# Performance work log

Measured on AMD Instinct MI355X. Metric: run time of the kernel, lower is better.

Reference implementation:

```python
import jax, jax.numpy as jnp
import numpy as np

B = 8192
D = 32
K = 8
H0 = 256
H1 = 256
PER = 3 * K + 1  # 25 params per dim
SCALE = 10.0
RMIN, RMAX = -SCALE / 2.0, SCALE / 2.0
MIN_BW = 1e-3; MIN_BH = 1e-3; MIN_KS = 1e-3
CUR_STEPS = 10000.0; CUR_START = 0.0
DX_MB = 1e-4   # distrax min_bin_size default
DX_MS = 1e-4   # distrax min_knot_slope default
DX_OFF = float(np.log(np.expm1(1.0 - DX_MS)))  # so softplus(0+off)+ms == 1


def _masks():
    deg_in = np.arange(1, D + 1)
    hd0 = np.arange(H0) % (D - 1) + 1
    hd1 = np.arange(H1) % (D - 1) + 1
    m0 = (hd0[:, None] >= deg_in[None, :]).astype(np.float32).T      # (D, H0)
    m1 = (hd1[:, None] >= hd0[None, :]).astype(np.float32).T        # (H0, H1)
    out_mask = (deg_in[:, None] > hd1[None, :]).astype(np.float32)  # (D, H1)
    per_mask = np.repeat(out_mask, PER, axis=0)                      # (D*PER, H1)
    return jnp.asarray(m0), jnp.asarray(m1), jnp.asarray(per_mask)

M0, M1, PER_MASK = _masks()


def made(y, W0, b0, W1, b1, W_out, b_out):
    h = jax.nn.gelu(y @ (W0 * M0) + b0)
    h = jax.nn.gelu(h @ (W1 * M1) + b1)
    proj = h @ (W_out.T * PER_MASK.T) + b_out  # (B, D*PER)
    return proj.reshape(y.shape[0], D, PER)


def _g(a, idx):
    return jnp.take_along_axis(a, idx[..., None], axis=-1)[..., 0]


def _knots(p, training_step):
    # module-level processing (rqs_from_params) ...
    w_raw, h_raw, s_raw = p[..., :K], p[..., K:2 * K], p[..., 2 * K:]
    lw = jax.nn.softmax(w_raw, axis=-1) * SCALE * (1.0 - K * MIN_BW) + MIN_BW
    lh = jax.nn.softmax(h_raw, axis=-1) * SCALE * (1.0 - K * MIN_BH) + MIN_BH
    ls = jax.nn.softplus(s_raw) + MIN_KS
    alpha = jnp.clip((jnp.asarray(training_step, jnp.float32) - CUR_START) / CUR_STEPS, 0.0, 1.0)
    bw = (1.0 - alpha) * (SCALE / K) + alpha * lw
    bh = (1.0 - alpha) * (SCALE / K) + alpha * lh
    sl = (1.0 - alpha) * 1.0 + alpha * ls
    bw = bw / jnp.sum(bw, axis=-1, keepdims=True) * SCALE
    bh = bh / jnp.sum(bh, axis=-1, keepdims=True) * SCALE
    # ... followed by distrax.RationalQuadraticSpline internal normalization
    widths = jax.nn.softmax(bw, axis=-1) * (SCALE - K * DX_MB) + DX_MB
    heights = jax.nn.softmax(bh, axis=-1) * (SCALE - K * DX_MB) + DX_MB
    slopes = jax.nn.softplus(sl + DX_OFF) + DX_MS  # (..., K+1)
    zpad = jnp.zeros_like(widths[..., :1])
    xp = RMIN + jnp.concatenate([zpad, jnp.cumsum(widths, axis=-1)], axis=-1)
    yp = RMIN + jnp.concatenate([zpad, jnp.cumsum(heights, axis=-1)], axis=-1)
    return xp, yp, widths, heights, slopes


def spline_fwd(p, x, training_step):
    xp, yp, w, h, d = _knots(p, training_step)
    inr = (x >= RMIN) & (x <= RMAX)
    xc = jnp.clip(x, RMIN, RMAX)
    idx = jnp.clip(jnp.sum((xc[..., None] >= xp[..., :-1]), axis=-1) - 1, 0, K - 1)
    xk, yk = _g(xp, idx), _g(yp, idx)
    wk, hk = _g(w, idx), _g(h, idx)
    dk, dk1 = _g(d, idx), _g(d, idx + 1)
    s = hk / wk
    xi = (xc - xk) / wk
    z1 = xi * (1.0 - xi)
    den = s + (dk1 + dk - 2.0 * s) * z1
    y = yk + hk * (s * xi * xi + dk * z1) / den
    ld = 2.0 * jnp.log(s) + jnp.log(dk1 * xi * xi + 2.0 * s * z1 + dk * (1.0 - xi) ** 2) - 2.0 * jnp.log(den)
    return jnp.where(inr, y, x), jnp.where(inr, ld, 0.0)


def spline_inv(p, y, training_step):
    xp, yp, w, h, d = _knots(p, training_step)
    inr = (y >= RMIN) & (y <= RMAX)
    yc = jnp.clip(y, RMIN, RMAX)
    idx = jnp.clip(jnp.sum((yc[..., None] >= yp[..., :-1]), axis=-1) - 1, 0, K - 1)
    xk, yk = _g(xp, idx), _g(yp, idx)
    wk, hk = _g(w, idx), _g(h, idx)
    dk, dk1 = _g(d, idx), _g(d, idx + 1)
    s = hk / wk
    t = yc - yk
    coef = dk1 + dk - 2.0 * s
    a = hk * (s - dk) + t * coef
    b = hk * dk - t * coef
    c = -s * t
    xi = 2.0 * c / (-b - jnp.sqrt(b * b - 4.0 * a * c))
    x = xi * wk + xk
    z1 = xi * (1.0 - xi)
    den = s + coef * z1
    ld = -(2.0 * jnp.log(s) + jnp.log(dk1 * xi * xi + 2.0 * s * z1 + dk * (1.0 - xi) ** 2) - 2.0 * jnp.log(den))
    return jnp.where(inr, x, y), jnp.where(inr, ld, 0.0)


def setup_inputs() -> dict:
    ks = jax.random.split(jax.random.key(0), 4)
    sd = lambda k, shp, fan: jax.random.normal(k, shp, jnp.float32) / np.sqrt(fan).astype(np.float32)
    return {
        "x": jax.random.normal(ks[0], (B, D), jnp.float32) * 1.5,
        "W0": sd(ks[1], (D, H0), D),
        "b0": jnp.zeros((H0,), jnp.float32),
        "W1": sd(ks[2], (H0, H1), H0),
        "b1": jnp.zeros((H1,), jnp.float32),
        "W_out": sd(ks[3], (D * PER, H1), H1),
        "b_out": jnp.zeros((D * PER,), jnp.float32),
        "forward": 0,
        "training_step": 10000,
    }


def reference(x, W0, b0, W1, b1, W_out, b_out, forward, training_step):
    if forward:
        p = made(x, W0, b0, W1, b1, W_out, b_out)  # (B, D, PER)
        z, ld = spline_fwd(p, x, training_step)
        return z, jnp.sum(ld, axis=1)
    z = x

    def body(carry, i):
        x_so, ldj = carry
        p = made(x_so, W0, b0, W1, b1, W_out, b_out)
        p_i = jax.lax.dynamic_index_in_dim(p, i, axis=1, keepdims=False)  # (B, PER)
        z_i = jax.lax.dynamic_index_in_dim(z, i, axis=1, keepdims=False)  # (B,)
        x_i, ld = spline_inv(p_i, z_i, training_step)
        return (x_so.at[:, i].set(x_i), ldj + ld), None

    init = (jnp.zeros_like(z), jnp.zeros((z.shape[0],), z.dtype))
    (x_fin, ldj), _ = jax.lax.scan(body, init, jnp.arange(D))
    return x_fin, ldj
```

## Files before the change

### kernel.cpp

```cpp
#include <hip/hip_runtime.h>

typedef _Float16 f16x8 __attribute__((ext_vector_type(8)));
typedef float f32x4 __attribute__((ext_vector_type(4)));

#define NB 8192
#define DD 32
#define PER 25
#define STRH 272

#define FENCE_C() do { asm volatile("" ::: "memory"); \
                       __builtin_amdgcn_sched_barrier(0); } while (0)
#define FENCE_HW() do { asm volatile("s_waitcnt lgkmcnt(0)" ::: "memory"); \
                        __builtin_amdgcn_sched_barrier(0); } while (0)

__device__ __forceinline__ float rcp_f(float x) { return __builtin_amdgcn_rcpf(x); }
__device__ __forceinline__ float gelu_f(float x) {
    float a = -1.5957691216057308f * (x + 0.044715f * x * x * x);
    return x * rcp_f(1.0f + __expf(a));
}
__device__ __forceinline__ float softplus_f(float x) {
    return (x > 20.0f) ? x : __logf(1.0f + __expf(x));
}
__device__ __forceinline__ int cntf(int d) {
    return (d <= 0) ? 0 : ((d <= 8) ? 9 * d : 72 + 8 * (d - 8));
}
__device__ __forceinline__ int porig(int u) {
    int d = (u < 72) ? (u / 9 + 1) : ((u - 72) / 8 + 9);
    int s = (u < 72) ? (u % 9) : ((u - 72) % 8);
    return s * 31 + (d - 1);
}

template<int CTRL>
__device__ __forceinline__ float qperm(float v) {
    return __int_as_float(__builtin_amdgcn_update_dpp(
        0, __float_as_int(v), CTRL, 0xF, 0xF, true));
}
__device__ __forceinline__ float qsum2(float v) {
    v += qperm<0xB1>(v);
    v += qperm<0x4E>(v);
    return v;
}
__device__ __forceinline__ float qmax2(float v) {
    v = fmaxf(v, qperm<0xB1>(v));
    v = fmaxf(v, qperm<0x4E>(v));
    return v;
}
__device__ __forceinline__ float qscan(float v, int p) {
    float t = qperm<0x90>(v);
    float c = v + ((p >= 1) ? t : 0.0f);
    float t2 = qperm<0x44>(c);
    return c + ((p >= 2) ? t2 : 0.0f);
}
__device__ __forceinline__ float sel4(float r0, float r1, float r2, float r3, int m) {
    float lo = (m & 1) ? r1 : r0;
    float hi = (m & 1) ? r3 : r2;
    return (m & 2) ? hi : lo;
}

__global__ void prep_kernel(const float* __restrict__ W0, const float* __restrict__ b0,
                            const float* __restrict__ W1, const float* __restrict__ b1,
                            const float* __restrict__ Wout, const float* __restrict__ bout,
                            _Float16* __restrict__ W0F, _Float16* __restrict__ W1F,
                            _Float16* __restrict__ WoutF,
                            float* __restrict__ b0F, float* __restrict__ b1F,
                            float* __restrict__ boutF)
{
    const int total = 16384 + 131072 + 262144 + 512 + 512 + 1024;
    for (int e = blockIdx.x * blockDim.x + threadIdx.x; e < total;
         e += gridDim.x * blockDim.x) {
        if (e < 16384) {
            int i = e >> 9, r = e & 511, lane = r >> 3, j = r & 7;
            int c = lane & 15, k = ((lane >> 4) << 3) + j;
            int nn = cntf(i) - cntf(i - 1);
            float v = 0.0f;
            if (c < nn && k < i) v = W0[k * 256 + (c * 31 + i - 1)];
            W0F[e] = (_Float16)v;
        } else if (e < 16384 + 131072) {
            int m = e - 16384;
            int i = m >> 12, r = m & 4095, kt = r >> 9, r2 = r & 511;
            int lane = r2 >> 3, j = r2 & 7;
            int c = lane & 15, kpos = kt * 32 + ((lane >> 4) << 3) + j;
            int nn = cntf(i) - cntf(i - 1), chi = cntf(i);
            float v = 0.0f;
            if (c < nn && kpos < chi) v = W1[porig(kpos) * 256 + (c * 31 + i - 1)];
            W1F[m] = (_Float16)v;
        } else if (e < 16384 + 131072 + 262144) {
            int m = e - (16384 + 131072);
            int i = m >> 13, r = m & 8191, ct = r >> 12, r2 = r & 4095;
            int kt = r2 >> 9, r3 = r2 & 511, lane = r3 >> 3, j = r3 & 7;
            int par = ct * 16 + (lane & 15), kpos = kt * 32 + ((lane >> 4) << 3) + j;
            int chi = cntf(i);
            float v = 0.0f;
            if (par < 25 && kpos < chi) v = Wout[(i * 25 + par) * 256 + porig(kpos)];
            WoutF[m] = (_Float16)v;
        } else if (e < 409600 + 512) {
            int m = e - 409600;
            int i = m >> 4, c = m & 15;
            int nn = cntf(i) - cntf(i - 1);
            b0F[m] = (c < nn) ? b0[c * 31 + i - 1] : 0.0f;
        } else if (e < 410112 + 512) {
            int m = e - 410112;
            int i = m >> 4, c = m & 15;
            int nn = cntf(i) - cntf(i - 1);
            b1F[m] = (c < nn) ? b1[c * 31 + i - 1] : 0.0f;
        } else {
            int m = e - 410624;
            int i = m >> 5, c = m & 31;
            boutF[m] = (c < 25) ? bout[i * 25 + c] : 0.0f;
        }
    }
}

__global__ __launch_bounds__(64, 1) void inv_kernel(
    const float* __restrict__ z,
    const _Float16* __restrict__ W0F, const _Float16* __restrict__ W1F,
    const _Float16* __restrict__ WoutF,
    const float* __restrict__ b0F, const float* __restrict__ b1F,
    const float* __restrict__ boutF,
    const int* __restrict__ tstep_p,
    float* __restrict__ xout, float* __restrict__ ldj)
{
    __shared__ float zs[16 * 33];
    __shared__ float xs[16 * 33];
    __shared__ float ps[16 * 33];
    __shared__ __align__(16) _Float16 h0L[16 * STRH];
    __shared__ __align__(16) _Float16 h1L[16 * STRH];

    const int l = threadIdx.x;
    const int c16 = l & 15;
    const int g = l >> 4;
    const int row0 = blockIdx.x * 16;

    for (int idx = l; idx < 512; idx += 64) {
        int r = idx >> 5, c = idx & 31;
        zs[r * 33 + c] = z[row0 * 32 + idx];
    }
    {
        unsigned int* p0 = (unsigned int*)h0L;
        unsigned int* p1 = (unsigned int*)h1L;
        for (int idx = l; idx < 16 * STRH / 2; idx += 64) { p0[idx] = 0u; p1[idx] = 0u; }
    }

    f16x8 xfrag;
#pragma unroll
    for (int j = 0; j < 8; ++j) xfrag[j] = (_Float16)0.0f;

    const float alpha = fminf(fmaxf(((float)(*tstep_p)) / 10000.0f, 0.0f), 1.0f);
    const float oma = 1.0f - alpha;
    const float dxoff = logf(expm1f(0.9999f));

    float ldreg = 0.0f;

    f16x8 wa2[2];
    float b0v2[2], b1v2[2], boA2[2], boB2[2];
    wa2[0] = *(const f16x8*)&W0F[l * 8];
    b0v2[0] = b0F[c16];
    b1v2[0] = b1F[c16];
    boA2[0] = boutF[c16];
    boB2[0] = boutF[16 + c16];

    FENCE_HW();

#pragma unroll 1
    for (int ib = 0; ib < DD; ib += 2) {
#pragma unroll
        for (int ph = 0; ph < 2; ++ph) {
            const int i = ib + ph;
            const int clo = cntf(i - 1);
            const int chi = cntf(i);
            const int nn = chi - clo;
            const int ip = (i + 1 < DD) ? (i + 1) : (DD - 1);

            wa2[ph ^ 1] = *(const f16x8*)&W0F[ip * 512 + l * 8];
            b0v2[ph ^ 1] = b0F[ip * 16 + c16];
            b1v2[ph ^ 1] = b1F[ip * 16 + c16];
            boA2[ph ^ 1] = boutF[ip * 32 + c16];
            boB2[ph ^ 1] = boutF[ip * 32 + 16 + c16];

            f16x8 wb_r[8], wc_r[2][8];
#pragma unroll
            for (int kt = 0; kt < 8; ++kt)
                wb_r[kt] = *(const f16x8*)&W1F[i * 4096 + kt * 512 + l * 8];
#pragma unroll
            for (int ct = 0; ct < 2; ++ct)
#pragma unroll
                for (int kt = 0; kt < 8; ++kt)
                    wc_r[ct][kt] = *(const f16x8*)&WoutF[i * 8192 + ct * 4096 + kt * 512 + l * 8];

            if (nn > 0) {
                f32x4 acc;
#pragma unroll
                for (int q = 0; q < 4; ++q) acc[q] = 0.0f;
                acc = __builtin_amdgcn_mfma_f32_16x16x32_f16(xfrag, wa2[ph], acc, 0, 0, 0);
                float bb = b0v2[ph];
                if (c16 < nn) {
                    const int col = clo + c16;
#pragma unroll
                    for (int q = 0; q < 4; ++q) {
                        int row = g * 4 + q;
                        int phys = (col & ~31) | ((col & 31) ^ (8 * (row & 3)));
                        h0L[row * STRH + phys] = (_Float16)gelu_f(acc[q] + bb);
                    }
                }
            }
            FENCE_HW();

            if (nn > 0) {
                const int fbase = c16 * STRH + ((g ^ (c16 & 3)) << 3);
                f32x4 acc;
#pragma unroll
                for (int q = 0; q < 4; ++q) acc[q] = 0.0f;
#pragma unroll
                for (int kt = 0; kt < 8; ++kt) {
                    if (kt * 32 < chi) {
                        f16x8 af = *(const f16x8*)&h0L[fbase + kt * 32];
                        acc = __builtin_amdgcn_mfma_f32_16x16x32_f16(af, wb_r[kt], acc, 0, 0, 0);
                    }
                }
                float bb = b1v2[ph];
                if (c16 < nn) {
                    const int col = clo + c16;
#pragma unroll
                    for (int q = 0; q < 4; ++q) {
                        int row = g * 4 + q;
                        int phys = (col & ~31) | ((col & 31) ^ (8 * (row & 3)));
                        h1L[row * STRH + phys] = (_Float16)gelu_f(acc[q] + bb);
                    }
                }
            }
            FENCE_HW();

            {
                const int fbase = c16 * STRH + ((g ^ (c16 & 3)) << 3);
                f32x4 acc0, acc1;
#pragma unroll
                for (int q = 0; q < 4; ++q) { acc0[q] = 0.0f; acc1[q] = 0.0f; }
#pragma unroll
                for (int kt = 0; kt < 8; ++kt) {
                    if (kt * 32 < chi) {
                        f16x8 af = *(const f16x8*)&h1L[fbase + kt * 32];
                        acc0 = __builtin_amdgcn_mfma_f32_16x16x32_f16(af, wc_r[0][kt], acc0, 0, 0, 0);
                        acc1 = __builtin_amdgcn_mfma_f32_16x16x32_f16(af, wc_r[1][kt], acc1, 0, 0, 0);
                    }
                }
                float boA = boA2[ph], boB = boB2[ph];
#pragma unroll
                for (int q = 0; q < 4; ++q)
                    ps[(g * 4 + q) * 33 + c16] = acc0[q] + boA;
                if (16 + c16 < 25) {
#pragma unroll
                    for (int q = 0; q < 4; ++q)
                        ps[(g * 4 + q) * 33 + 16 + c16] = acc1[q] + boB;
                }
            }
            FENCE_HW();

            float xv_sel;
            {
                const int r4 = l >> 2;
                const int p  = l & 3;

                const float* bp = &ps[r4 * 33];
                float w_a = bp[p],      w_b = bp[4 + p];
                float h_a = bp[8 + p],  h_b = bp[12 + p];
                float d_a = bp[16 + p], d_b = bp[20 + p], d_cin = bp[24];
                const float zi = zs[r4 * 33 + i];

                float m_w = qmax2(fmaxf(w_a, w_b));
                float ewa = __expf(w_a - m_w), ewb = __expf(w_b - m_w);
                float rsw = rcp_f(qsum2(ewa + ewb));
                float bwa = oma * 1.25f + alpha * (ewa * rsw * 9.92f + 0.001f);
                float bwb = oma * 1.25f + alpha * (ewb * rsw * 9.92f + 0.001f);
                float scw = 10.0f * rcp_f(qsum2(bwa + bwb));
                bwa *= scw; bwb *= scw;
                float e2wa = __expf(bwa), e2wb = __expf(bwb);
                float rs2w = rcp_f(qsum2(e2wa + e2wb));
                float wdt_a = e2wa * rs2w * 9.9992f + 1e-4f;
                float wdt_b = e2wb * rs2w * 9.9992f + 1e-4f;

                float m_h = qmax2(fmaxf(h_a, h_b));
                float eha = __expf(h_a - m_h), ehb = __expf(h_b - m_h);
                float rsh = rcp_f(qsum2(eha + ehb));
                float bha = oma * 1.25f + alpha * (eha * rsh * 9.92f + 0.001f);
                float bhb = oma * 1.25f + alpha * (ehb * rsh * 9.92f + 0.001f);
                float sch = 10.0f * rcp_f(qsum2(bha + bhb));
                bha *= sch; bhb *= sch;
                float e2ha = __expf(bha), e2hb = __expf(bhb);
                float rs2h = rcp_f(qsum2(e2ha + e2hb));
                float hgt_a = e2ha * rs2h * 9.9992f + 1e-4f;
                float hgt_b = e2hb * rs2h * 9.9992f + 1e-4f;

                float dsl_a = softplus_f(oma + alpha * (softplus_f(d_a) + 0.001f) + dxoff) + 1e-4f;
                float dsl_b = softplus_f(oma + alpha * (softplus_f(d_b) + 0.001f) + dxoff) + 1e-4f;
                float dsl_c = softplus_f(oma + alpha * (softplus_f(d_cin) + 0.001f) + dxoff) + 1e-4f;

                float ca  = qscan(wdt_a, p);
                float cb  = qscan(wdt_b, p) + qperm<0xFF>(ca);
                float cha = qscan(hgt_a, p);
                float chb = qscan(hgt_b, p) + qperm<0xFF>(cha);

                float wdA1 = qperm<0xB1>(wdt_a), wdA2 = qperm<0x4E>(wdt_a), wdA3 = qperm<0x1B>(wdt_a);
                float wdB1 = qperm<0xB1>(wdt_b), wdB2 = qperm<0x4E>(wdt_b), wdB3 = qperm<0x1B>(wdt_b);
                float hgA1 = qperm<0xB1>(hgt_a), hgA2 = qperm<0x4E>(hgt_a), hgA3 = qperm<0x1B>(hgt_a);
                float hgB1 = qperm<0xB1>(hgt_b), hgB2 = qperm<0x4E>(hgt_b), hgB3 = qperm<0x1B>(hgt_b);
                float dsA1 = qperm<0xB1>(dsl_a), dsA2 = qperm<0x4E>(dsl_a), dsA3 = qperm<0x1B>(dsl_a);
                float dsB1 = qperm<0xB1>(dsl_b), dsB2 = qperm<0x4E>(dsl_b), dsB3 = qperm<0x1B>(dsl_b);
                float caA1 = qperm<0xB1>(ca),    caA2 = qperm<0x4E>(ca),    caA3 = qperm<0x1B>(ca);
                float caB1 = qperm<0xB1>(cb),    caB2 = qperm<0x4E>(cb),    caB3 = qperm<0x1B>(cb);
                float chA1 = qperm<0xB1>(cha),   chA2 = qperm<0x4E>(cha),   chA3 = qperm<0x1B>(cha);
                float chB1 = qperm<0xB1>(chb),   chB2 = qperm<0x4E>(chb),   chB3 = qperm<0x1B>(chb);

                const bool inr = (zi >= -5.0f) && (zi <= 5.0f);
                const float yc = fminf(fmaxf(zi, -5.0f), 5.0f);

                float ch7 = qperm<0xFF>(chb);
                int cnt = 0;
                cnt += (yc >= cha  - 5.0f); cnt += (yc >= chA1 - 5.0f);
                cnt += (yc >= chA2 - 5.0f); cnt += (yc >= chA3 - 5.0f);
                cnt += (yc >= chb  - 5.0f); cnt += (yc >= chB1 - 5.0f);
                cnt += (yc >= chB2 - 5.0f); cnt += (yc >= chB3 - 5.0f);
                int idx = cnt - ((yc >= ch7 - 5.0f) ? 1 : 0);

                int mA = (idx & 3) ^ p;
                bool hiH = (idx >= 4);
                float wk = hiH ? sel4(wdt_b, wdB1, wdB2, wdB3, mA)
                               : sel4(wdt_a, wdA1, wdA2, wdA3, mA);
                float hk = hiH ? sel4(hgt_b, hgB1, hgB2, hgB3, mA)
                               : sel4(hgt_a, hgA1, hgA2, hgA3, mA);
                float dk = hiH ? sel4(dsl_b, dsB1, dsB2, dsB3, mA)
                               : sel4(dsl_a, dsA1, dsA2, dsA3, mA);
                int j1 = idx + 1;
                int mJ = (j1 & 3) ^ p;
                float d1A = sel4(dsl_a, dsA1, dsA2, dsA3, mJ);
                float d1B = sel4(dsl_b, dsB1, dsB2, dsB3, mJ);
                float dk1 = (j1 < 4) ? d1A : ((j1 < 8) ? d1B : dsl_c);
                int im1 = idx - 1;
                int mM = (im1 & 3) ^ p;
                float cwm = (im1 < 4) ? sel4(ca, caA1, caA2, caA3, mM)
                                      : sel4(cb, caB1, caB2, caB3, mM);
                float chm = (im1 < 4) ? sel4(cha, chA1, chA2, chA3, mM)
                                      : sel4(chb, chB1, chB2, chB3, mM);
                float xk = (idx == 0) ? -5.0f : (cwm - 5.0f);
                float yk = (idx == 0) ? -5.0f : (chm - 5.0f);

                float s_ = hk * rcp_f(wk);
                float tt = yc - yk;
                float coef = dk1 + dk - 2.0f * s_;
                float aa = hk * (s_ - dk) + tt * coef;
                float bb = hk * dk - tt * coef;
                float cc = -s_ * tt;
                float disc = bb * bb - 4.0f * aa * cc;
                float xi = 2.0f * cc * rcp_f(-bb - __builtin_amdgcn_sqrtf(disc));
                float xv = xi * wk + xk;
                float z1 = xi * (1.0f - xi);
                float den = s_ + coef * z1;
                float omxi = 1.0f - xi;
                float num = dk1 * xi * xi + 2.0f * s_ * z1 + dk * omxi * omxi;
                float ld = __logf(den * den * rcp_f(s_ * s_ * num));

                xv_sel = inr ? xv : zi;
                ldreg += inr ? ld : 0.0f;
                if (p == 0) xs[r4 * 33 + i] = xv_sel;
            }

            {
                float xnew = __shfl(xv_sel, (l & 15) << 2);
                if (g == (i >> 3)) {
#pragma unroll
                    for (int j = 0; j < 8; ++j)
                        if (j == (i & 7)) xfrag[j] = (_Float16)xnew;
                }
            }
            FENCE_C();
        }
    }

    FENCE_HW();
    for (int idx = l; idx < 512; idx += 64) {
        int r = idx >> 5, c = idx & 31;
        xout[row0 * 32 + idx] = xs[r * 33 + c];
    }
    if ((l & 3) == 0) ldj[row0 + (l >> 2)] = ldreg;
}

extern "C" void kernel_launch(void* const* d_in, const int* in_sizes, int n_in,
                              void* d_out, int out_size, void* d_ws, size_t ws_size,
                              hipStream_t stream)
{
    const float* z    = (const float*)d_in[0];
    const float* W0   = (const float*)d_in[1];
    const float* b0   = (const float*)d_in[2];
    const float* W1   = (const float*)d_in[3];
    const float* b1   = (const float*)d_in[4];
    const float* Wout = (const float*)d_in[5];
    const float* bout = (const float*)d_in[6];
    const int* tstep  = (const int*)d_in[8];

    float* out  = (float*)d_out;
    float* xout = out;
    float* ldj  = out + NB * DD;

    _Float16* W0F   = (_Float16*)d_ws;
    _Float16* W1F   = W0F + 16384;
    _Float16* WoutF = W1F + 131072;
    float* b0F  = (float*)(WoutF + 262144);
    float* b1F  = b0F + 512;
    float* boutF = b1F + 512;

    prep_kernel<<<1608, 256, 0, stream>>>(W0, b0, W1, b1, Wout, bout,
                                          W0F, W1F, WoutF, b0F, b1F, boutF);
    inv_kernel<<<NB / 16, 64, 0, stream>>>(z, W0F, W1F, WoutF, b0F, b1F, boutF,
                                           tstep, xout, ldj);
}
```

Before: 83.79 us.

## Precompute next step's first-layer MFMA early and add newest x contribution as rank-1 update

The first-layer MFMA for step i+1 is now issued during step i, before the spline stage, using the x fragment that does not yet hold x_i. The missing x_i term is added later as a scalar FMA with the raw fp32 W0 weight, which is loaded separately. This takes the layer-0 MFMA off the serial critical path between the spline result and the next layer. The cost is an extra global load and shuffles per step, and the newest term is now added in fp32 rather than fp16.

```diff
diff --git a/kernel.cpp b/kernel.cpp
--- a/kernel.cpp
+++ b/kernel.cpp
@@ -112,7 +112,7 @@
 }
 
 __global__ __launch_bounds__(64, 1) void inv_kernel(
-    const float* __restrict__ z,
+    const float* __restrict__ z, const float* __restrict__ W0raw,
     const _Float16* __restrict__ W0F, const _Float16* __restrict__ W1F,
     const _Float16* __restrict__ WoutF,
     const float* __restrict__ b0F, const float* __restrict__ b1F,
@@ -153,11 +153,17 @@
 
     f16x8 wa2[2];
     float b0v2[2], b1v2[2], boA2[2], boB2[2];
+    float w0i2[2];
+    f32x4 accA;
+    f32x4 xi4;
     wa2[0] = *(const f16x8*)&W0F[l * 8];
     b0v2[0] = b0F[c16];
     b1v2[0] = b1F[c16];
     boA2[0] = boutF[c16];
     boB2[0] = boutF[16 + c16];
+    w0i2[0] = 0.0f;
+#pragma unroll
+    for (int q = 0; q < 4; ++q) { accA[q] = 0.0f; xi4[q] = 0.0f; }
 
     FENCE_HW();
 
@@ -171,11 +177,18 @@
             const int nn = chi - clo;
             const int ip = (i + 1 < DD) ? (i + 1) : (DD - 1);
 
+            const float zi = zs[(l >> 2) * 33 + i];
+
             wa2[ph ^ 1] = *(const f16x8*)&W0F[ip * 512 + l * 8];
             b0v2[ph ^ 1] = b0F[ip * 16 + c16];
             b1v2[ph ^ 1] = b1F[ip * 16 + c16];
             boA2[ph ^ 1] = boutF[ip * 32 + c16];
             boB2[ph ^ 1] = boutF[ip * 32 + 16 + c16];
+            {
+                int widx = c16 * 31 + i;
+                widx = (widx > 255) ? 255 : widx;
+                w0i2[ph ^ 1] = W0raw[i * 256 + widx];
+            }
 
             f16x8 wb_r[8], wc_r[2][8];
 #pragma unroll
@@ -188,18 +201,16 @@
                     wc_r[ct][kt] = *(const f16x8*)&WoutF[i * 8192 + ct * 4096 + kt * 512 + l * 8];
 
             if (nn > 0) {
-                f32x4 acc;
-#pragma unroll
-                for (int q = 0; q < 4; ++q) acc[q] = 0.0f;
-                acc = __builtin_amdgcn_mfma_f32_16x16x32_f16(xfrag, wa2[ph], acc, 0, 0, 0);
                 float bb = b0v2[ph];
+                float w0i = w0i2[ph];
                 if (c16 < nn) {
                     const int col = clo + c16;
 #pragma unroll
                     for (int q = 0; q < 4; ++q) {
+                        float v = accA[q] + xi4[q] * w0i + bb;
                         int row = g * 4 + q;
                         int phys = (col & ~31) | ((col & 31) ^ (8 * (row & 3)));
-                        h0L[row * STRH + phys] = (_Float16)gelu_f(acc[q] + bb);
+                        h0L[row * STRH + phys] = (_Float16)gelu_f(v);
                     }
                 }
             }
@@ -253,6 +264,13 @@
                         ps[(g * 4 + q) * 33 + 16 + c16] = acc1[q] + boB;
                 }
             }
+
+            {
+                f32x4 zz;
+#pragma unroll
+                for (int q = 0; q < 4; ++q) zz[q] = 0.0f;
+                accA = __builtin_amdgcn_mfma_f32_16x16x32_f16(xfrag, wa2[ph ^ 1], zz, 0, 0, 0);
+            }
             FENCE_HW();
 
             float xv_sel;
@@ -264,7 +282,6 @@
                 float w_a = bp[p],      w_b = bp[4 + p];
                 float h_a = bp[8 + p],  h_b = bp[12 + p];
                 float d_a = bp[16 + p], d_b = bp[20 + p], d_cin = bp[24];
-                const float zi = zs[r4 * 33 + i];
 
                 float m_w = qmax2(fmaxf(w_a, w_b));
                 float ewa = __expf(w_a - m_w), ewb = __expf(w_b - m_w);
@@ -360,10 +377,13 @@
 
                 xv_sel = inr ? xv : zi;
                 ldreg += inr ? ld : 0.0f;
-                if (p == 0) xs[r4 * 33 + i] = xv_sel;
+                if (p == 0) xs[(l >> 2) * 33 + i] = xv_sel;
             }
 
             {
+#pragma unroll
+                for (int q = 0; q < 4; ++q)
+                    xi4[q] = __shfl(xv_sel, (g * 4 + q) << 2);
                 float xnew = __shfl(xv_sel, (l & 15) << 2);
                 if (g == (i >> 3)) {
 #pragma unroll
@@ -409,6 +429,6 @@
 
     prep_kernel<<<1608, 256, 0, stream>>>(W0, b0, W1, b1, Wout, bout,
                                           W0F, W1F, WoutF, b0F, b1F, boutF);
-    inv_kernel<<<NB / 16, 64, 0, stream>>>(z, W0F, W1F, WoutF, b0F, b1F, boutF,
+    inv_kernel<<<NB / 16, 64, 0, stream>>>(z, W0, W0F, W1F, WoutF, b0F, b1F, boutF,
                                            tstep, xout, ldj);
 }
```

Result: no change. 82.85 us, median of 2 (-1.1%).
